# Kernel optimization log

Measured on AMD Instinct MI355X. Metric: run time of the kernel, lower is better.

Reference implementation:

```python
import jax, jax.numpy as jnp
import numpy as np

N, E, F_IN, HID, HEADS, OUT = 50000, 800000, 128, 64, 4, 40


def gat_layer(x, src, dst, n, W, a_src, a_dst, b, heads, ch):
    # PyG GATConv: h = x @ W per head; e_ij = LeakyReLU(a_src.h_j + a_dst.h_i)
    h = (x @ W).reshape(n, heads, ch)
    al_s = jnp.einsum('nhc,hc->nh', h, a_src)  # source-side logit term
    al_d = jnp.einsum('nhc,hc->nh', h, a_dst)  # target-side logit term
    e = jax.nn.leaky_relu(al_s[src] + al_d[dst], negative_slope=0.2)  # [E,H]
    m = jax.ops.segment_max(e, dst, num_segments=n)  # stable softmax per target node
    e = jnp.exp(e - m[dst])
    s = jax.ops.segment_sum(e, dst, num_segments=n)
    alpha = e / s[dst]  # [E,H]
    out = jax.ops.segment_sum(h[src] * alpha[:, :, None], dst, num_segments=n)  # [n,H,C]
    return out.reshape(n, heads * ch) + b


def gat_forward(x, src, dst, W0, as0, ad0, b0, W1, as1, ad1, b1, W2, as2, ad2, b2):
    n = x.shape[0]
    x = jax.nn.elu(gat_layer(x, src, dst, n, W0, as0, ad0, b0, HEADS, HID))
    x = jax.nn.elu(gat_layer(x, src, dst, n, W1, as1, ad1, b1, HEADS, HID))
    x = gat_layer(x, src, dst, n, W2, as2, ad2, b2, 1, OUT)
    return jax.nn.log_softmax(x, axis=1)


def setup_inputs() -> dict:
    key = jax.random.key(0)
    ks = jax.random.split(key, 16)
    x = jax.random.normal(ks[0], (N, F_IN), dtype=jnp.float32)
    edge_index = jax.random.randint(ks[1], (2, E), 0, N, dtype=jnp.int64)
    g = lambda k, sh: jax.random.normal(k, sh, dtype=jnp.float32) * (1.0 / np.sqrt(sh[0]))
    d_hid = HID * HEADS
    return {
        'x': x, 'edge_index': edge_index,
        'W0': g(ks[2], (F_IN, d_hid)), 'as0': g(ks[3], (HEADS, HID)), 'ad0': g(ks[4], (HEADS, HID)), 'b0': jnp.zeros((d_hid,), jnp.float32),
        'W1': g(ks[5], (d_hid, d_hid)), 'as1': g(ks[6], (HEADS, HID)), 'ad1': g(ks[7], (HEADS, HID)), 'b1': jnp.zeros((d_hid,), jnp.float32),
        'W2': g(ks[8], (d_hid, OUT)), 'as2': g(ks[9], (1, OUT)), 'ad2': g(ks[10], (1, OUT)), 'b2': jnp.zeros((OUT,), jnp.float32),
    }


def reference(x, edge_index, W0, as0, ad0, b0, W1, as1, ad1, b1, W2, as2, ad2, b2):
    n = x.shape[0]
    loops = jnp.arange(n, dtype=edge_index.dtype)  # PyG add_self_loops=True
    src = jnp.concatenate([edge_index[0], loops])
    dst = jnp.concatenate([edge_index[1], loops])
    return gat_forward(x, src, dst, W0, as0, ad0, b0, W1, as1, ad1, b1, W2, as2, ad2, b2)
```

## Files before the change

kernel.cpp:

```cpp
#include <hip/hip_runtime.h>
#include <hip/hip_fp16.h>
#include <math.h>

#define NODES 50000
#define NEDGES 800000
#define TOT_E (NEDGES + NODES)
#define SCAN_B 256
#define SCAN_NB ((NODES + SCAN_B - 1) / SCAN_B)

typedef __attribute__((ext_vector_type(8))) _Float16 half8v;
typedef __attribute__((ext_vector_type(4))) float f32x4;

union U2H { uint u; __half2 h; };

static __device__ __forceinline__ float lrelu(float z) {
  return z > 0.f ? z : 0.2f * z;
}
static __device__ __forceinline__ ushort f2h(float f) {
  __half h = __float2half_rn(f);
  return *reinterpret_cast<ushort*>(&h);
}
static __device__ __forceinline__ void wave_lds_fence() {
  __builtin_amdgcn_wave_barrier();
  asm volatile("s_waitcnt lgkmcnt(0)" ::: "memory");
  __builtin_amdgcn_sched_barrier(0);
}

static __device__ __forceinline__ void packB_one(const float* __restrict__ W,
    ushort* __restrict__ Bp, int N, int NF, int idx) {
  int i = idx & 7;
  int lane = (idx >> 3) & 63;
  int rem = idx >> 9;
  int nf = rem % NF;
  int kf = rem / NF;
  int k = kf * 32 + (lane >> 4) * 8 + i;
  int col = nf * 16 + (lane & 15);
  float v = (col < N) ? W[(size_t)k * N + col] : 0.f;
  Bp[idx] = f2h(v);
}

__global__ __launch_bounds__(256) void k_setup(const int* __restrict__ dst,
    int* __restrict__ counts, const float* __restrict__ x, ushort* __restrict__ xb0,
    const float* __restrict__ W0, ushort* __restrict__ Bp0,
    const float* __restrict__ W1, ushort* __restrict__ Bp1,
    const float* __restrict__ W2, ushort* __restrict__ Bp2) {
  int gb = blockIdx.x;
  int tid = threadIdx.x;
  if (gb < 2048) {
    int stride = 2048 * 256;
    for (int i = gb * 256 + tid; i < TOT_E; i += stride) {
      int d = (i < NEDGES) ? dst[i] : (i - NEDGES);
      atomicAdd(&counts[d], 1);
    }
  } else if (gb < 4048) {
    int total4 = NODES * 128 / 4;
    int stride = 2000 * 256;
    for (int i = (gb - 2048) * 256 + tid; i < total4; i += stride) {
      float4 v = *(const float4*)&x[i * 4];
      ushort4 o;
      o.x = f2h(v.x); o.y = f2h(v.y); o.z = f2h(v.z); o.w = f2h(v.w);
      *(ushort4*)&xb0[i * 4] = o;
    }
  } else {
    int b = gb - 4048;
    int stride = 48 * 256;
    int base = b * 256 + tid;
    for (int idx = base; idx < 4 * 16 * 512; idx += stride) packB_one(W0, Bp0, 256, 16, idx);
    for (int idx = base; idx < 8 * 16 * 512; idx += stride) packB_one(W1, Bp1, 256, 16, idx);
    for (int idx = base; idx < 8 * 3 * 512; idx += stride)  packB_one(W2, Bp2, 40, 3, idx);
  }
}

__global__ __launch_bounds__(SCAN_B) void k_scan_red_part(const int* __restrict__ counts,
    int* __restrict__ bsum, int* __restrict__ bpre, int* __restrict__ done) {
  __shared__ int sm[SCAN_B];
  __shared__ int lastflag;
  int idx = blockIdx.x * SCAN_B + threadIdx.x;
  int v = (idx < NODES) ? counts[idx] : 0;
  sm[threadIdx.x] = v;
  __syncthreads();
  for (int off = SCAN_B / 2; off > 0; off >>= 1) {
    if (threadIdx.x < off) sm[threadIdx.x] += sm[threadIdx.x + off];
    __syncthreads();
  }
  if (threadIdx.x == 0) {
    __hip_atomic_store(&bsum[blockIdx.x], sm[0], __ATOMIC_RELEASE, __HIP_MEMORY_SCOPE_AGENT);
    int t = __hip_atomic_fetch_add(done, 1, __ATOMIC_ACQ_REL, __HIP_MEMORY_SCOPE_AGENT);
    lastflag = (t == (int)gridDim.x - 1);
  }
  __syncthreads();
  if (!lastflag) return;
  int tid = threadIdx.x;
  int b = (tid < SCAN_NB)
      ? __hip_atomic_load(&bsum[tid], __ATOMIC_ACQUIRE, __HIP_MEMORY_SCOPE_AGENT) : 0;
  __syncthreads();
  sm[tid] = b;
  __syncthreads();
  for (int off = 1; off < 256; off <<= 1) {
    int t2 = (tid >= off) ? sm[tid - off] : 0;
    __syncthreads();
    sm[tid] += t2;
    __syncthreads();
  }
  if (tid < SCAN_NB) bpre[tid] = sm[tid] - b;
}

__global__ __launch_bounds__(SCAN_B) void k_scan_emit(const int* __restrict__ counts,
    const int* __restrict__ bpre, int* __restrict__ offs, int* __restrict__ cur) {
  __shared__ int sm[SCAN_B];
  int idx = blockIdx.x * SCAN_B + threadIdx.x;
  int tid = threadIdx.x;
  int v = (idx < NODES) ? counts[idx] : 0;
  sm[tid] = v;
  __syncthreads();
  for (int off = 1; off < SCAN_B; off <<= 1) {
    int t = (tid >= off) ? sm[tid - off] : 0;
    __syncthreads();
    sm[tid] += t;
    __syncthreads();
  }
  int base = bpre[blockIdx.x];
  int excl = base + sm[tid] - v;
  if (idx < NODES) { offs[idx] = excl; cur[idx] = excl; }
  if (idx == NODES - 1) offs[NODES] = excl + v;
}

__global__ void k_scatter(const int* __restrict__ src, const int* __restrict__ dst,
                          int* __restrict__ cur, ushort* __restrict__ ssrc) {
  int stride = gridDim.x * blockDim.x;
  for (int i = blockIdx.x * blockDim.x + threadIdx.x; i < TOT_E; i += stride) {
    int s, d;
    if (i < NEDGES) { s = src[i]; d = dst[i]; } else { s = i - NEDGES; d = s; }
    int pos = atomicAdd(&cur[d], 1);
    ssrc[pos] = (ushort)s;
  }
}

template<int KF, int NFW, int CG, int HEADS, int NF_TOT>
__global__ __launch_bounds__(256, 2) void k_gemm_reg(
    const ushort* __restrict__ A, const ushort* __restrict__ Bp,
    ushort* __restrict__ H, const float* __restrict__ a_s, const float* __restrict__ a_d,
    float* __restrict__ al_s, float* __restrict__ al_d, int M, int N, int K) {
  int wib = threadIdx.x >> 6;
  int lane = threadIdx.x & 63;
  int lg = lane >> 4;
  int lr = lane & 15;
  int cg, strip0, sstride;
  if (CG == 4) { cg = wib; strip0 = blockIdx.x; sstride = gridDim.x; }
  else { cg = 0; strip0 = blockIdx.x * 4 + wib; sstride = gridDim.x * 4; }

  half8v b[KF][NFW];
#pragma unroll
  for (int kf = 0; kf < KF; ++kf)
#pragma unroll
    for (int n = 0; n < NFW; ++n)
      b[kf][n] = *(const half8v*)(Bp + ((size_t)(kf * NF_TOT + cg * NFW + n) * 64 + lane) * 8);

  float asc[NFW], adc[NFW];
#pragma unroll
  for (int n = 0; n < NFW; ++n) {
    int col = (cg * NFW + n) * 16 + lr;
    bool ok = col < N;
    asc[n] = ok ? a_s[col] : 0.f;
    adc[n] = ok ? a_d[col] : 0.f;
  }

  int nstrips = M >> 4;
  for (int strip = strip0; strip < nstrips; strip += sstride) {
    const ushort* arow = A + (size_t)(strip * 16 + lr) * K + lg * 8;
    half8v a[KF];
#pragma unroll
    for (int kf = 0; kf < KF; ++kf) a[kf] = *(const half8v*)(arow + kf * 32);
    f32x4 acc[NFW];
#pragma unroll
    for (int n = 0; n < NFW; ++n) acc[n] = (f32x4){0.f, 0.f, 0.f, 0.f};
#pragma unroll
    for (int kf = 0; kf < KF; ++kf)
#pragma unroll
      for (int n = 0; n < NFW; ++n)
        acc[n] = __builtin_amdgcn_mfma_f32_16x16x32_f16(a[kf], b[kf][n], acc[n], 0, 0, 0);

#pragma unroll
    for (int n = 0; n < NFW; ++n) {
      int col = (cg * NFW + n) * 16 + lr;
      if (col < N) {
#pragma unroll
        for (int r = 0; r < 4; ++r) {
          int row = strip * 16 + lg * 4 + r;
          H[(size_t)row * N + col] = f2h(acc[n][r]);
        }
      }
    }

    float ps[4], pd[4];
#pragma unroll
    for (int r = 0; r < 4; ++r) {
      float s = 0.f, d = 0.f;
#pragma unroll
      for (int n = 0; n < NFW; ++n) {
        s += acc[n][r] * asc[n];
        d += acc[n][r] * adc[n];
      }
      ps[r] = s; pd[r] = d;
    }
#pragma unroll
    for (int off = 1; off <= 8; off <<= 1)
#pragma unroll
      for (int t = 0; t < 4; ++t) {
        ps[t] += __shfl_xor(ps[t], off);
        pd[t] += __shfl_xor(pd[t], off);
      }
    if (lr < 4) {
      int row = strip * 16 + lg * 4 + lr;
      if (HEADS == 4) {
        al_s[row * 4 + cg] = ps[lr];
        al_d[row * 4 + cg] = pd[lr];
      } else {
        al_s[row] = ps[lr];
        al_d[row] = pd[lr];
      }
    }
  }
}

__global__ __launch_bounds__(256) void k_agg4(const ushort* __restrict__ hb,
    const float* __restrict__ al_s, const float* __restrict__ al_d,
    const int* __restrict__ offs, const ushort* __restrict__ ssrc,
    const float* __restrict__ bias, ushort* __restrict__ outb) {
  __shared__ uint s_sv[8][32];
  __shared__ uint s_al[8][4][33];
  int hw = threadIdx.x >> 5;
  int node = (blockIdx.x * 256 + threadIdx.x) >> 5;
  if (node >= NODES) return;
  int l = threadIdx.x & 31;
  int beg = offs[node], end = offs[node + 1];
  float4 ald4 = *(const float4*)&al_d[node * 4];

  float m[4] = {-1e30f, -1e30f, -1e30f, -1e30f};
  for (int i = beg + l; i < end; i += 32) {
    int sv = ssrc[i];
    float4 a4 = *(const float4*)&al_s[sv * 4];
    m[0] = fmaxf(m[0], lrelu(a4.x + ald4.x));
    m[1] = fmaxf(m[1], lrelu(a4.y + ald4.y));
    m[2] = fmaxf(m[2], lrelu(a4.z + ald4.z));
    m[3] = fmaxf(m[3], lrelu(a4.w + ald4.w));
  }
#pragma unroll
  for (int off = 1; off <= 16; off <<= 1) {
#pragma unroll
    for (int h = 0; h < 4; ++h) m[h] = fmaxf(m[h], __shfl_xor(m[h], off));
  }

  int hh = l >> 3;
  uint clb = (uint)l * 8;
  float sacc[4] = {0.f, 0.f, 0.f, 0.f};
  __half2 z2 = __float2half2_rn(0.f);
  __half2 accA[4] = {z2, z2, z2, z2};
  __half2 accB[4] = {z2, z2, z2, z2};

  for (int cb = beg; cb < end; cb += 32) {
    int cnt = min(32, end - cb);
    wave_lds_fence();
    if (l < cnt) {
      uint sv = (uint)ssrc[cb + l];
      float4 a4 = *(const float4*)&al_s[sv * 4];
      float t0 = __expf(lrelu(a4.x + ald4.x) - m[0]);
      float t1 = __expf(lrelu(a4.y + ald4.y) - m[1]);
      float t2 = __expf(lrelu(a4.z + ald4.z) - m[2]);
      float t3 = __expf(lrelu(a4.w + ald4.w) - m[3]);
      sacc[0] += t0; sacc[1] += t1; sacc[2] += t2; sacc[3] += t3;
      U2H p0, p1, p2, p3;
      p0.h = __float2half2_rn(t0); p1.h = __float2half2_rn(t1);
      p2.h = __float2half2_rn(t2); p3.h = __float2half2_rn(t3);
      s_sv[hw][l] = sv;
      s_al[hw][0][l] = p0.u; s_al[hw][1][l] = p1.u;
      s_al[hw][2][l] = p2.u; s_al[hw][3][l] = p3.u;
    }
    wave_lds_fence();
    int e = 0;
    for (; e + 7 < cnt; e += 8) {
      uint sv0 = s_sv[hw][e],     sv1 = s_sv[hw][e + 1];
      uint sv2 = s_sv[hw][e + 2], sv3 = s_sv[hw][e + 3];
      uint sv4 = s_sv[hw][e + 4], sv5 = s_sv[hw][e + 5];
      uint sv6 = s_sv[hw][e + 6], sv7 = s_sv[hw][e + 7];
      U2H a0, a1, a2, a3, a4, a5, a6, a7;
      a0.u = s_al[hw][hh][e];     a1.u = s_al[hw][hh][e + 1];
      a2.u = s_al[hw][hh][e + 2]; a3.u = s_al[hw][hh][e + 3];
      a4.u = s_al[hw][hh][e + 4]; a5.u = s_al[hw][hh][e + 5];
      a6.u = s_al[hw][hh][e + 6]; a7.u = s_al[hw][hh][e + 7];
      uint4 hv0 = *(const uint4*)(hb + ((sv0 << 8) + clb));
      uint4 hv1 = *(const uint4*)(hb + ((sv1 << 8) + clb));
      uint4 hv2 = *(const uint4*)(hb + ((sv2 << 8) + clb));
      uint4 hv3 = *(const uint4*)(hb + ((sv3 << 8) + clb));
      uint4 hv4 = *(const uint4*)(hb + ((sv4 << 8) + clb));
      uint4 hv5 = *(const uint4*)(hb + ((sv5 << 8) + clb));
      uint4 hv6 = *(const uint4*)(hb + ((sv6 << 8) + clb));
      uint4 hv7 = *(const uint4*)(hb + ((sv7 << 8) + clb));
      U2H v;
      v.u = hv0.x; accA[0] = __hfma2(a0.h, v.h, accA[0]);
      v.u = hv0.y; accA[1] = __hfma2(a0.h, v.h, accA[1]);
      v.u = hv0.z; accA[2] = __hfma2(a0.h, v.h, accA[2]);
      v.u = hv0.w; accA[3] = __hfma2(a0.h, v.h, accA[3]);
      v.u = hv1.x; accB[0] = __hfma2(a1.h, v.h, accB[0]);
      v.u = hv1.y; accB[1] = __hfma2(a1.h, v.h, accB[1]);
      v.u = hv1.z; accB[2] = __hfma2(a1.h, v.h, accB[2]);
      v.u = hv1.w; accB[3] = __hfma2(a1.h, v.h, accB[3]);
      v.u = hv2.x; accA[0] = __hfma2(a2.h, v.h, accA[0]);
      v.u = hv2.y; accA[1] = __hfma2(a2.h, v.h, accA[1]);
      v.u = hv2.z; accA[2] = __hfma2(a2.h, v.h, accA[2]);
      v.u = hv2.w; accA[3] = __hfma2(a2.h, v.h, accA[3]);
      v.u = hv3.x; accB[0] = __hfma2(a3.h, v.h, accB[0]);
      v.u = hv3.y; accB[1] = __hfma2(a3.h, v.h, accB[1]);
      v.u = hv3.z; accB[2] = __hfma2(a3.h, v.h, accB[2]);
      v.u = hv3.w; accB[3] = __hfma2(a3.h, v.h, accB[3]);
      v.u = hv4.x; accA[0] = __hfma2(a4.h, v.h, accA[0]);
      v.u = hv4.y; accA[1] = __hfma2(a4.h, v.h, accA[1]);
      v.u = hv4.z; accA[2] = __hfma2(a4.h, v.h, accA[2]);
      v.u = hv4.w; accA[3] = __hfma2(a4.h, v.h, accA[3]);
      v.u = hv5.x; accB[0] = __hfma2(a5.h, v.h, accB[0]);
      v.u = hv5.y; accB[1] = __hfma2(a5.h, v.h, accB[1]);
      v.u = hv5.z; accB[2] = __hfma2(a5.h, v.h, accB[2]);
      v.u = hv5.w; accB[3] = __hfma2(a5.h, v.h, accB[3]);
      v.u = hv6.x; accA[0] = __hfma2(a6.h, v.h, accA[0]);
      v.u = hv6.y; accA[1] = __hfma2(a6.h, v.h, accA[1]);
      v.u = hv6.z; accA[2] = __hfma2(a6.h, v.h, accA[2]);
      v.u = hv6.w; accA[3] = __hfma2(a6.h, v.h, accA[3]);
      v.u = hv7.x; accB[0] = __hfma2(a7.h, v.h, accB[0]);
      v.u = hv7.y; accB[1] = __hfma2(a7.h, v.h, accB[1]);
      v.u = hv7.z; accB[2] = __hfma2(a7.h, v.h, accB[2]);
      v.u = hv7.w; accB[3] = __hfma2(a7.h, v.h, accB[3]);
    }
    for (; e + 3 < cnt; e += 4) {
      uint sv0 = s_sv[hw][e],     sv1 = s_sv[hw][e + 1];
      uint sv2 = s_sv[hw][e + 2], sv3 = s_sv[hw][e + 3];
      U2H a0, a1, a2, a3;
      a0.u = s_al[hw][hh][e];     a1.u = s_al[hw][hh][e + 1];
      a2.u = s_al[hw][hh][e + 2]; a3.u = s_al[hw][hh][e + 3];
      uint4 hv0 = *(const uint4*)(hb + ((sv0 << 8) + clb));
      uint4 hv1 = *(const uint4*)(hb + ((sv1 << 8) + clb));
      uint4 hv2 = *(const uint4*)(hb + ((sv2 << 8) + clb));
      uint4 hv3 = *(const uint4*)(hb + ((sv3 << 8) + clb));
      U2H v;
      v.u = hv0.x; accA[0] = __hfma2(a0.h, v.h, accA[0]);
      v.u = hv0.y; accA[1] = __hfma2(a0.h, v.h, accA[1]);
      v.u = hv0.z; accA[2] = __hfma2(a0.h, v.h, accA[2]);
      v.u = hv0.w; accA[3] = __hfma2(a0.h, v.h, accA[3]);
      v.u = hv1.x; accB[0] = __hfma2(a1.h, v.h, accB[0]);
      v.u = hv1.y; accB[1] = __hfma2(a1.h, v.h, accB[1]);
      v.u = hv1.z; accB[2] = __hfma2(a1.h, v.h, accB[2]);
      v.u = hv1.w; accB[3] = __hfma2(a1.h, v.h, accB[3]);
      v.u = hv2.x; accA[0] = __hfma2(a2.h, v.h, accA[0]);
      v.u = hv2.y; accA[1] = __hfma2(a2.h, v.h, accA[1]);
      v.u = hv2.z; accA[2] = __hfma2(a2.h, v.h, accA[2]);
      v.u = hv2.w; accA[3] = __hfma2(a2.h, v.h, accA[3]);
      v.u = hv3.x; accB[0] = __hfma2(a3.h, v.h, accB[0]);
      v.u = hv3.y; accB[1] = __hfma2(a3.h, v.h, accB[1]);
      v.u = hv3.z; accB[2] = __hfma2(a3.h, v.h, accB[2]);
      v.u = hv3.w; accB[3] = __hfma2(a3.h, v.h, accB[3]);
    }
    for (; e < cnt; ++e) {
      uint sv = s_sv[hw][e];
      U2H a0; a0.u = s_al[hw][hh][e];
      uint4 hv = *(const uint4*)(hb + ((sv << 8) + clb));
      U2H v;
      v.u = hv.x; accA[0] = __hfma2(a0.h, v.h, accA[0]);
      v.u = hv.y; accA[1] = __hfma2(a0.h, v.h, accA[1]);
      v.u = hv.z; accA[2] = __hfma2(a0.h, v.h, accA[2]);
      v.u = hv.w; accA[3] = __hfma2(a0.h, v.h, accA[3]);
    }
  }
#pragma unroll
  for (int off = 1; off <= 16; off <<= 1) {
#pragma unroll
    for (int h = 0; h < 4; ++h) sacc[h] += __shfl_xor(sacc[h], off);
  }
  float invs = 1.f / sacc[hh];
  ushort4 ores[2];
#pragma unroll
  for (int j = 0; j < 4; ++j) {
    U2H t; t.h = __hadd2(accA[j], accB[j]);
    float lo = __low2float(t.h) * invs + bias[l * 8 + j * 2];
    float hi = __high2float(t.h) * invs + bias[l * 8 + j * 2 + 1];
    lo = lo > 0.f ? lo : __expf(lo) - 1.f;
    hi = hi > 0.f ? hi : __expf(hi) - 1.f;
    ((ushort*)ores)[j * 2]     = f2h(lo);
    ((ushort*)ores)[j * 2 + 1] = f2h(hi);
  }
  *(ushort4*)(outb + (size_t)node * 256 + l * 8)     = ores[0];
  *(ushort4*)(outb + (size_t)node * 256 + l * 8 + 4) = ores[1];
}

__global__ __launch_bounds__(256) void k_agg1(const ushort* __restrict__ hb,
    const float* __restrict__ al_s, const float* __restrict__ al_d,
    const int* __restrict__ offs, const ushort* __restrict__ ssrc,
    const float* __restrict__ bias, float* __restrict__ out) {
  __shared__ uint s_sv[8][32];
  __shared__ uint s_al[8][32];
  int hw = threadIdx.x >> 5;
  int node = (blockIdx.x * 256 + threadIdx.x) >> 5;
  if (node >= NODES) return;
  int l = threadIdx.x & 31;
  int beg = offs[node], end = offs[node + 1];
  float ald = al_d[node];

  float m = -1e30f;
  for (int i = beg + l; i < end; i += 32)
    m = fmaxf(m, lrelu(al_s[ssrc[i]] + ald));
#pragma unroll
  for (int off = 1; off <= 16; off <<= 1) m = fmaxf(m, __shfl_xor(m, off));

  int p = l >> 4;
  int cq = l & 15;
  bool act = cq < 10;
  uint cqb = (uint)cq * 4;
  float sacc = 0.f;
  __half2 z2 = __float2half2_rn(0.f);
  __half2 accA[2] = {z2, z2};
  __half2 accB[2] = {z2, z2};
  for (int cb = beg; cb < end; cb += 32) {
    int cnt = min(32, end - cb);
    wave_lds_fence();
    if (l < cnt) {
      uint sv = (uint)ssrc[cb + l];
      float t = __expf(lrelu(al_s[sv] + ald) - m);
      sacc += t;
      U2H pk; pk.h = __float2half2_rn(t);
      s_sv[hw][l] = sv;
      s_al[hw][l] = pk.u;
    }
    wave_lds_fence();
    int e = p;
    for (; e + 14 < cnt; e += 16) {
      uint sv0 = s_sv[hw][e],      sv1 = s_sv[hw][e + 2];
      uint sv2 = s_sv[hw][e + 4],  sv3 = s_sv[hw][e + 6];
      uint sv4 = s_sv[hw][e + 8],  sv5 = s_sv[hw][e + 10];
      uint sv6 = s_sv[hw][e + 12], sv7 = s_sv[hw][e + 14];
      U2H a0, a1, a2, a3, a4, a5, a6, a7;
      a0.u = s_al[hw][e];      a1.u = s_al[hw][e + 2];
      a2.u = s_al[hw][e + 4];  a3.u = s_al[hw][e + 6];
      a4.u = s_al[hw][e + 8];  a5.u = s_al[hw][e + 10];
      a6.u = s_al[hw][e + 12]; a7.u = s_al[hw][e + 14];
      if (act) {
        uint2 hv0 = *(const uint2*)(hb + (sv0 * 40u + cqb));
        uint2 hv1 = *(const uint2*)(hb + (sv1 * 40u + cqb));
        uint2 hv2 = *(const uint2*)(hb + (sv2 * 40u + cqb));
        uint2 hv3 = *(const uint2*)(hb + (sv3 * 40u + cqb));
        uint2 hv4 = *(const uint2*)(hb + (sv4 * 40u + cqb));
        uint2 hv5 = *(const uint2*)(hb + (sv5 * 40u + cqb));
        uint2 hv6 = *(const uint2*)(hb + (sv6 * 40u + cqb));
        uint2 hv7 = *(const uint2*)(hb + (sv7 * 40u + cqb));
        U2H v;
        v.u = hv0.x; accA[0] = __hfma2(a0.h, v.h, accA[0]);
        v.u = hv0.y; accA[1] = __hfma2(a0.h, v.h, accA[1]);
        v.u = hv1.x; accB[0] = __hfma2(a1.h, v.h, accB[0]);
        v.u = hv1.y; accB[1] = __hfma2(a1.h, v.h, accB[1]);
        v.u = hv2.x; accA[0] = __hfma2(a2.h, v.h, accA[0]);
        v.u = hv2.y; accA[1] = __hfma2(a2.h, v.h, accA[1]);
        v.u = hv3.x; accB[0] = __hfma2(a3.h, v.h, accB[0]);
        v.u = hv3.y; accB[1] = __hfma2(a3.h, v.h, accB[1]);
        v.u = hv4.x; accA[0] = __hfma2(a4.h, v.h, accA[0]);
        v.u = hv4.y; accA[1] = __hfma2(a4.h, v.h, accA[1]);
        v.u = hv5.x; accB[0] = __hfma2(a5.h, v.h, accB[0]);
        v.u = hv5.y; accB[1] = __hfma2(a5.h, v.h, accB[1]);
        v.u = hv6.x; accA[0] = __hfma2(a6.h, v.h, accA[0]);
        v.u = hv6.y; accA[1] = __hfma2(a6.h, v.h, accA[1]);
        v.u = hv7.x; accB[0] = __hfma2(a7.h, v.h, accB[0]);
        v.u = hv7.y; accB[1] = __hfma2(a7.h, v.h, accB[1]);
      }
    }
    for (; e + 6 < cnt; e += 8) {
      uint sv0 = s_sv[hw][e],     sv1 = s_sv[hw][e + 2];
      uint sv2 = s_sv[hw][e + 4], sv3 = s_sv[hw][e + 6];
      U2H a0, a1, a2, a3;
      a0.u = s_al[hw][e];     a1.u = s_al[hw][e + 2];
      a2.u = s_al[hw][e + 4]; a3.u = s_al[hw][e + 6];
      if (act) {
        uint2 hv0 = *(const uint2*)(hb + (sv0 * 40u + cqb));
        uint2 hv1 = *(const uint2*)(hb + (sv1 * 40u + cqb));
        uint2 hv2 = *(const uint2*)(hb + (sv2 * 40u + cqb));
        uint2 hv3 = *(const uint2*)(hb + (sv3 * 40u + cqb));
        U2H v;
        v.u = hv0.x; accA[0] = __hfma2(a0.h, v.h, accA[0]);
        v.u = hv0.y; accA[1] = __hfma2(a0.h, v.h, accA[1]);
        v.u = hv1.x; accB[0] = __hfma2(a1.h, v.h, accB[0]);
        v.u = hv1.y; accB[1] = __hfma2(a1.h, v.h, accB[1]);
        v.u = hv2.x; accA[0] = __hfma2(a2.h, v.h, accA[0]);
        v.u = hv2.y; accA[1] = __hfma2(a2.h, v.h, accA[1]);
        v.u = hv3.x; accB[0] = __hfma2(a3.h, v.h, accB[0]);
        v.u = hv3.y; accB[1] = __hfma2(a3.h, v.h, accB[1]);
      }
    }
    for (; e < cnt; e += 2) {
      uint sv = s_sv[hw][e];
      U2H a0; a0.u = s_al[hw][e];
      if (act) {
        uint2 hv = *(const uint2*)(hb + (sv * 40u + cqb));
        U2H v;
        v.u = hv.x; accA[0] = __hfma2(a0.h, v.h, accA[0]);
        v.u = hv.y; accA[1] = __hfma2(a0.h, v.h, accA[1]);
      }
    }
  }
#pragma unroll
  for (int off = 1; off <= 16; off <<= 1) sacc += __shfl_xor(sacc, off);
  float invs = 1.f / sacc;
  float vv[4];
#pragma unroll
  for (int j = 0; j < 2; ++j) {
    U2H t; t.h = __hadd2(accA[j], accB[j]);
    U2H o; o.u = __shfl_xor(t.u, 16);
    t.h = __hadd2(t.h, o.h);
    vv[j * 2]     = __low2float(t.h) * invs;
    vv[j * 2 + 1] = __high2float(t.h) * invs;
  }
  float mm = -1e30f;
  if (act) {
#pragma unroll
    for (int j = 0; j < 4; ++j) {
      vv[j] += bias[cq * 4 + j];
      mm = fmaxf(mm, vv[j]);
    }
  }
#pragma unroll
  for (int off = 1; off <= 8; off <<= 1) mm = fmaxf(mm, __shfl_xor(mm, off));
  float se = 0.f;
  if (act) {
#pragma unroll
    for (int j = 0; j < 4; ++j) se += __expf(vv[j] - mm);
  }
#pragma unroll
  for (int off = 1; off <= 8; off <<= 1) se += __shfl_xor(se, off);
  if (act && p == 0) {
    float lse = mm + __logf(se);
    float4 o;
    o.x = vv[0] - lse; o.y = vv[1] - lse; o.z = vv[2] - lse; o.w = vv[3] - lse;
    *(float4*)&out[(size_t)node * 40 + cq * 4] = o;
  }
}

extern "C" void kernel_launch(void* const* d_in, const int* in_sizes, int n_in,
                              void* d_out, int out_size, void* d_ws, size_t ws_size,
                              hipStream_t stream) {
  const float* x   = (const float*)d_in[0];
  const int*   ei  = (const int*)d_in[1];
  const float* W0  = (const float*)d_in[2];
  const float* as0 = (const float*)d_in[3];
  const float* ad0 = (const float*)d_in[4];
  const float* b0  = (const float*)d_in[5];
  const float* W1  = (const float*)d_in[6];
  const float* as1 = (const float*)d_in[7];
  const float* ad1 = (const float*)d_in[8];
  const float* b1  = (const float*)d_in[9];
  const float* W2  = (const float*)d_in[10];
  const float* as2 = (const float*)d_in[11];
  const float* ad2 = (const float*)d_in[12];
  const float* b2  = (const float*)d_in[13];
  float* out = (float*)d_out;

  char* p = (char*)d_ws;
  auto take = [&](size_t bytes) {
    char* q = p;
    p += (bytes + 255) & ~(size_t)255;
    return (void*)q;
  };
  ushort* xb0 = (ushort*)take((size_t)NODES * 128 * 2);
  ushort* xb1 = (ushort*)take((size_t)NODES * 256 * 2);
  ushort* xb2 = (ushort*)take((size_t)NODES * 256 * 2);
  ushort* hb  = (ushort*)take((size_t)NODES * 256 * 2);
  float* als  = (float*)take((size_t)NODES * 4 * 4);
  float* ald  = (float*)take((size_t)NODES * 4 * 4);
  ushort* ssrc= (ushort*)take((size_t)TOT_E * 2);
  int* offs   = (int*)take((size_t)(NODES + 1) * 4);
  int* cur    = (int*)take((size_t)NODES * 4);
  int* cnt    = (int*)take((size_t)(NODES + 64) * 4);
  int* done   = cnt + NODES;
  int* bsum   = (int*)take((size_t)SCAN_NB * 4);
  int* bpre   = (int*)take((size_t)SCAN_NB * 4);
  ushort* Bp0 = (ushort*)take((size_t)4 * 16 * 512 * 2);
  ushort* Bp1 = (ushort*)take((size_t)8 * 16 * 512 * 2);
  ushort* Bp2 = (ushort*)take((size_t)8 * 3 * 512 * 2);

  hipMemsetAsync(cnt, 0, (size_t)(NODES + 64) * 4, stream);
  k_setup<<<4096, 256, 0, stream>>>(ei + NEDGES, cnt, x, xb0, W0, Bp0, W1, Bp1, W2, Bp2);
  k_scan_red_part<<<SCAN_NB, SCAN_B, 0, stream>>>(cnt, bsum, bpre, done);
  k_scan_emit<<<SCAN_NB, SCAN_B, 0, stream>>>(cnt, bpre, offs, cur);
  k_scatter<<<4096, 256, 0, stream>>>(ei, ei + NEDGES, cur, ssrc);

  int nab = (NODES * 32 + 255) / 256;

  k_gemm_reg<4, 4, 4, 4, 16><<<512, 256, 0, stream>>>(xb0, Bp0, hb, as0, ad0, als, ald, NODES, 256, 128);
  k_agg4<<<nab, 256, 0, stream>>>(hb, als, ald, offs, ssrc, b0, xb1);

  k_gemm_reg<8, 4, 4, 4, 16><<<512, 256, 0, stream>>>(xb1, Bp1, hb, as1, ad1, als, ald, NODES, 256, 256);
  k_agg4<<<nab, 256, 0, stream>>>(hb, als, ald, offs, ssrc, b1, xb2);

  k_gemm_reg<8, 3, 1, 1, 3><<<512, 256, 0, stream>>>(xb2, Bp2, hb, as2, ad2, als, ald, NODES, 40, 256);
  k_agg1<<<nab, 256, 0, stream>>>(hb, als, ald, offs, ssrc, b2, out);
}
```

Before: 296.2 us.

## Split 4-head aggregation into head-pair blocks mapped per XCD

The 4-head aggregation kernel now launches twice as many blocks. Each block handles one pair of heads (128 channels) for eight nodes, and the pair is chosen from the block index's XCD bits so that each XCD's L2 caches only half of every feature row. Within a wave, the two 16-lane halves process alternating edges and combine their partial sums with a lane shuffle before writing. The intent is to shrink each XCD's gather working set and improve L2 hit rate. The cost is that the softmax max/sum pass over edges is repeated for each head pair, and only half the lanes store results.

```diff
diff --git a/kernel.cpp b/kernel.cpp
--- a/kernel.cpp
+++ b/kernel.cpp
@@ -228,32 +228,36 @@
     const int* __restrict__ offs, const ushort* __restrict__ ssrc,
     const float* __restrict__ bias, ushort* __restrict__ outb) {
   __shared__ uint s_sv[8][32];
-  __shared__ uint s_al[8][4][33];
+  __shared__ uint s_al[8][2][33];
+  int bid = blockIdx.x;
+  int xcd = bid & 7;
+  int hp = xcd >> 2;
+  int nb = (bid >> 3) * 4 + (xcd & 3);
   int hw = threadIdx.x >> 5;
-  int node = (blockIdx.x * 256 + threadIdx.x) >> 5;
+  int node = nb * 8 + hw;
   if (node >= NODES) return;
   int l = threadIdx.x & 31;
   int beg = offs[node], end = offs[node + 1];
-  float4 ald4 = *(const float4*)&al_d[node * 4];
-
-  float m[4] = {-1e30f, -1e30f, -1e30f, -1e30f};
+  float2 ald2 = *(const float2*)&al_d[node * 4 + hp * 2];
+
+  float m0 = -1e30f, m1 = -1e30f;
   for (int i = beg + l; i < end; i += 32) {
     int sv = ssrc[i];
-    float4 a4 = *(const float4*)&al_s[sv * 4];
-    m[0] = fmaxf(m[0], lrelu(a4.x + ald4.x));
-    m[1] = fmaxf(m[1], lrelu(a4.y + ald4.y));
-    m[2] = fmaxf(m[2], lrelu(a4.z + ald4.z));
-    m[3] = fmaxf(m[3], lrelu(a4.w + ald4.w));
+    float2 a2 = *(const float2*)&al_s[sv * 4 + hp * 2];
+    m0 = fmaxf(m0, lrelu(a2.x + ald2.x));
+    m1 = fmaxf(m1, lrelu(a2.y + ald2.y));
   }
 #pragma unroll
   for (int off = 1; off <= 16; off <<= 1) {
-#pragma unroll
-    for (int h = 0; h < 4; ++h) m[h] = fmaxf(m[h], __shfl_xor(m[h], off));
-  }
-
-  int hh = l >> 3;
-  uint clb = (uint)l * 8;
-  float sacc[4] = {0.f, 0.f, 0.f, 0.f};
+    m0 = fmaxf(m0, __shfl_xor(m0, off));
+    m1 = fmaxf(m1, __shfl_xor(m1, off));
+  }
+
+  int e = l >> 4;
+  int c = l & 15;
+  int hsel = c >> 3;
+  uint clb = (uint)(hp * 128 + c * 8);
+  float sacc0 = 0.f, sacc1 = 0.f;
   __half2 z2 = __float2half2_rn(0.f);
   __half2 accA[4] = {z2, z2, z2, z2};
   __half2 accB[4] = {z2, z2, z2, z2};
@@ -263,79 +267,23 @@
     wave_lds_fence();
     if (l < cnt) {
       uint sv = (uint)ssrc[cb + l];
-      float4 a4 = *(const float4*)&al_s[sv * 4];
-      float t0 = __expf(lrelu(a4.x + ald4.x) - m[0]);
-      float t1 = __expf(lrelu(a4.y + ald4.y) - m[1]);
-      float t2 = __expf(lrelu(a4.z + ald4.z) - m[2]);
-      float t3 = __expf(lrelu(a4.w + ald4.w) - m[3]);
-      sacc[0] += t0; sacc[1] += t1; sacc[2] += t2; sacc[3] += t3;
-      U2H p0, p1, p2, p3;
+      float2 a2 = *(const float2*)&al_s[sv * 4 + hp * 2];
+      float t0 = __expf(lrelu(a2.x + ald2.x) - m0);
+      float t1 = __expf(lrelu(a2.y + ald2.y) - m1);
+      sacc0 += t0; sacc1 += t1;
+      U2H p0, p1;
       p0.h = __float2half2_rn(t0); p1.h = __float2half2_rn(t1);
-      p2.h = __float2half2_rn(t2); p3.h = __float2half2_rn(t3);
       s_sv[hw][l] = sv;
       s_al[hw][0][l] = p0.u; s_al[hw][1][l] = p1.u;
-      s_al[hw][2][l] = p2.u; s_al[hw][3][l] = p3.u;
     }
     wave_lds_fence();
-    int e = 0;
-    for (; e + 7 < cnt; e += 8) {
-      uint sv0 = s_sv[hw][e],     sv1 = s_sv[hw][e + 1];
-      uint sv2 = s_sv[hw][e + 2], sv3 = s_sv[hw][e + 3];
-      uint sv4 = s_sv[hw][e + 4], sv5 = s_sv[hw][e + 5];
-      uint sv6 = s_sv[hw][e + 6], sv7 = s_sv[hw][e + 7];
-      U2H a0, a1, a2, a3, a4, a5, a6, a7;
-      a0.u = s_al[hw][hh][e];     a1.u = s_al[hw][hh][e + 1];
-      a2.u = s_al[hw][hh][e + 2]; a3.u = s_al[hw][hh][e + 3];
-      a4.u = s_al[hw][hh][e + 4]; a5.u = s_al[hw][hh][e + 5];
-      a6.u = s_al[hw][hh][e + 6]; a7.u = s_al[hw][hh][e + 7];
-      uint4 hv0 = *(const uint4*)(hb + ((sv0 << 8) + clb));
-      uint4 hv1 = *(const uint4*)(hb + ((sv1 << 8) + clb));
-      uint4 hv2 = *(const uint4*)(hb + ((sv2 << 8) + clb));
-      uint4 hv3 = *(const uint4*)(hb + ((sv3 << 8) + clb));
-      uint4 hv4 = *(const uint4*)(hb + ((sv4 << 8) + clb));
-      uint4 hv5 = *(const uint4*)(hb + ((sv5 << 8) + clb));
-      uint4 hv6 = *(const uint4*)(hb + ((sv6 << 8) + clb));
-      uint4 hv7 = *(const uint4*)(hb + ((sv7 << 8) + clb));
-      U2H v;
-      v.u = hv0.x; accA[0] = __hfma2(a0.h, v.h, accA[0]);
-      v.u = hv0.y; accA[1] = __hfma2(a0.h, v.h, accA[1]);
-      v.u = hv0.z; accA[2] = __hfma2(a0.h, v.h, accA[2]);
-      v.u = hv0.w; accA[3] = __hfma2(a0.h, v.h, accA[3]);
-      v.u = hv1.x; accB[0] = __hfma2(a1.h, v.h, accB[0]);
-      v.u = hv1.y; accB[1] = __hfma2(a1.h, v.h, accB[1]);
-      v.u = hv1.z; accB[2] = __hfma2(a1.h, v.h, accB[2]);
-      v.u = hv1.w; accB[3] = __hfma2(a1.h, v.h, accB[3]);
-      v.u = hv2.x; accA[0] = __hfma2(a2.h, v.h, accA[0]);
-      v.u = hv2.y; accA[1] = __hfma2(a2.h, v.h, accA[1]);
-      v.u = hv2.z; accA[2] = __hfma2(a2.h, v.h, accA[2]);
-      v.u = hv2.w; accA[3] = __hfma2(a2.h, v.h, accA[3]);
-      v.u = hv3.x; accB[0] = __hfma2(a3.h, v.h, accB[0]);
-      v.u = hv3.y; accB[1] = __hfma2(a3.h, v.h, accB[1]);
-      v.u = hv3.z; accB[2] = __hfma2(a3.h, v.h, accB[2]);
-      v.u = hv3.w; accB[3] = __hfma2(a3.h, v.h, accB[3]);
-      v.u = hv4.x; accA[0] = __hfma2(a4.h, v.h, accA[0]);
-      v.u = hv4.y; accA[1] = __hfma2(a4.h, v.h, accA[1]);
-      v.u = hv4.z; accA[2] = __hfma2(a4.h, v.h, accA[2]);
-      v.u = hv4.w; accA[3] = __hfma2(a4.h, v.h, accA[3]);
-      v.u = hv5.x; accB[0] = __hfma2(a5.h, v.h, accB[0]);
-      v.u = hv5.y; accB[1] = __hfma2(a5.h, v.h, accB[1]);
-      v.u = hv5.z; accB[2] = __hfma2(a5.h, v.h, accB[2]);
-      v.u = hv5.w; accB[3] = __hfma2(a5.h, v.h, accB[3]);
-      v.u = hv6.x; accA[0] = __hfma2(a6.h, v.h, accA[0]);
-      v.u = hv6.y; accA[1] = __hfma2(a6.h, v.h, accA[1]);
-      v.u = hv6.z; accA[2] = __hfma2(a6.h, v.h, accA[2]);
-      v.u = hv6.w; accA[3] = __hfma2(a6.h, v.h, accA[3]);
-      v.u = hv7.x; accB[0] = __hfma2(a7.h, v.h, accB[0]);
-      v.u = hv7.y; accB[1] = __hfma2(a7.h, v.h, accB[1]);
-      v.u = hv7.z; accB[2] = __hfma2(a7.h, v.h, accB[2]);
-      v.u = hv7.w; accB[3] = __hfma2(a7.h, v.h, accB[3]);
-    }
-    for (; e + 3 < cnt; e += 4) {
-      uint sv0 = s_sv[hw][e],     sv1 = s_sv[hw][e + 1];
-      uint sv2 = s_sv[hw][e + 2], sv3 = s_sv[hw][e + 3];
+    int ee = e;
+    for (; ee + 6 < cnt; ee += 8) {
+      uint sv0 = s_sv[hw][ee],     sv1 = s_sv[hw][ee + 2];
+      uint sv2 = s_sv[hw][ee + 4], sv3 = s_sv[hw][ee + 6];
       U2H a0, a1, a2, a3;
-      a0.u = s_al[hw][hh][e];     a1.u = s_al[hw][hh][e + 1];
-      a2.u = s_al[hw][hh][e + 2]; a3.u = s_al[hw][hh][e + 3];
+      a0.u = s_al[hw][hsel][ee];     a1.u = s_al[hw][hsel][ee + 2];
+      a2.u = s_al[hw][hsel][ee + 4]; a3.u = s_al[hw][hsel][ee + 6];
       uint4 hv0 = *(const uint4*)(hb + ((sv0 << 8) + clb));
       uint4 hv1 = *(const uint4*)(hb + ((sv1 << 8) + clb));
       uint4 hv2 = *(const uint4*)(hb + ((sv2 << 8) + clb));
@@ -358,9 +306,9 @@
       v.u = hv3.z; accB[2] = __hfma2(a3.h, v.h, accB[2]);
       v.u = hv3.w; accB[3] = __hfma2(a3.h, v.h, accB[3]);
     }
-    for (; e < cnt; ++e) {
-      uint sv = s_sv[hw][e];
-      U2H a0; a0.u = s_al[hw][hh][e];
+    for (; ee < cnt; ee += 2) {
+      uint sv = s_sv[hw][ee];
+      U2H a0; a0.u = s_al[hw][hsel][ee];
       uint4 hv = *(const uint4*)(hb + ((sv << 8) + clb));
       U2H v;
       v.u = hv.x; accA[0] = __hfma2(a0.h, v.h, accA[0]);
@@ -371,23 +319,27 @@
   }
 #pragma unroll
   for (int off = 1; off <= 16; off <<= 1) {
-#pragma unroll
-    for (int h = 0; h < 4; ++h) sacc[h] += __shfl_xor(sacc[h], off);
-  }
-  float invs = 1.f / sacc[hh];
+    sacc0 += __shfl_xor(sacc0, off);
+    sacc1 += __shfl_xor(sacc1, off);
+  }
+  float invs = 1.f / (hsel ? sacc1 : sacc0);
   ushort4 ores[2];
 #pragma unroll
   for (int j = 0; j < 4; ++j) {
     U2H t; t.h = __hadd2(accA[j], accB[j]);
-    float lo = __low2float(t.h) * invs + bias[l * 8 + j * 2];
-    float hi = __high2float(t.h) * invs + bias[l * 8 + j * 2 + 1];
+    U2H o; o.u = __shfl_xor(t.u, 16);
+    t.h = __hadd2(t.h, o.h);
+    float lo = __low2float(t.h) * invs + bias[clb + j * 2];
+    float hi = __high2float(t.h) * invs + bias[clb + j * 2 + 1];
     lo = lo > 0.f ? lo : __expf(lo) - 1.f;
     hi = hi > 0.f ? hi : __expf(hi) - 1.f;
     ((ushort*)ores)[j * 2]     = f2h(lo);
     ((ushort*)ores)[j * 2 + 1] = f2h(hi);
   }
-  *(ushort4*)(outb + (size_t)node * 256 + l * 8)     = ores[0];
-  *(ushort4*)(outb + (size_t)node * 256 + l * 8 + 4) = ores[1];
+  if (e == 0) {
+    *(ushort4*)(outb + (size_t)node * 256 + clb)     = ores[0];
+    *(ushort4*)(outb + (size_t)node * 256 + clb + 4) = ores[1];
+  }
 }
 
 __global__ __launch_bounds__(256) void k_agg1(const ushort* __restrict__ hb,
@@ -587,12 +539,14 @@
   k_scatter<<<4096, 256, 0, stream>>>(ei, ei + NEDGES, cur, ssrc);
 
   int nab = (NODES * 32 + 255) / 256;
+  int nab4 = (nab + 3) & ~3;
+  int nagg4 = nab4 * 2;
 
   k_gemm_reg<4, 4, 4, 4, 16><<<512, 256, 0, stream>>>(xb0, Bp0, hb, as0, ad0, als, ald, NODES, 256, 128);
-  k_agg4<<<nab, 256, 0, stream>>>(hb, als, ald, offs, ssrc, b0, xb1);
+  k_agg4<<<nagg4, 256, 0, stream>>>(hb, als, ald, offs, ssrc, b0, xb1);
 
   k_gemm_reg<8, 4, 4, 4, 16><<<512, 256, 0, stream>>>(xb1, Bp1, hb, as1, ad1, als, ald, NODES, 256, 256);
-  k_agg4<<<nab, 256, 0, stream>>>(hb, als, ald, offs, ssrc, b1, xb2);
+  k_agg4<<<nagg4, 256, 0, stream>>>(hb, als, ald, offs, ssrc, b1, xb2);
 
   k_gemm_reg<8, 3, 1, 1, 3><<<512, 256, 0, stream>>>(xb2, Bp2, hb, as2, ad2, als, ald, NODES, 40, 256);
   k_agg1<<<nab, 256, 0, stream>>>(hb, als, ald, offs, ssrc, b2, out);
```

Result: faster. 287.9 us (median of 2 runs) (-2.8%).
